# Optimization experiments

Hardware: AMD Instinct MI355X
Metric: run time of the kernel (lower is better)

Reference implementation:

```python
import jax, jax.numpy as jnp
import numpy as np

CONTEXT = 5
PAD = CONTEXT // 2
EPS = 1e-12  # torch F.normalize eps


def _conv2d(x, w, b):
    # x: [B,Cin,H,W], w: [Cout,Cin,3,3], SAME padding (pad=1)
    y = jax.lax.conv_general_dilated(
        x, w, window_strides=(1, 1), padding='SAME',
        dimension_numbers=('NCHW', 'OIHW', 'NCHW'))
    return y + b[None, :, None, None]


def _self_similarity(fn):
    # fn: L2-normalized features [B,C,H,W] -> cost volume [B,25,H,W]
    b, c, h, w = fn.shape
    fp = jnp.pad(fn, ((0, 0), (0, 0), (PAD, PAD), (PAD, PAD)))
    # channel index = col*CONTEXT + row, matching the torch loop order
    planes = [
        (fp[:, :, r:h + r, cc:w + cc] * fn).sum(axis=1)
        for cc in range(CONTEXT) for r in range(CONTEXT)
    ]
    return jnp.stack(planes, axis=1)


def setup_inputs() -> dict:
    key = jax.random.key(0)
    ks = jax.random.split(key, 5)
    B, C, H, W = 8, 512, 96, 96
    OC = 128
    return {
        'feature': jax.random.normal(ks[0], (B, C, H, W), dtype=jnp.float32),
        'w0': jax.random.normal(ks[1], (2 * OC, CONTEXT * CONTEXT, 3, 3), dtype=jnp.float32) * 0.05,
        'b0': jax.random.normal(ks[2], (2 * OC,), dtype=jnp.float32) * 0.01,
        'w1': jax.random.normal(ks[3], (OC, 2 * OC, 3, 3), dtype=jnp.float32) * 0.05,
        'b1': jax.random.normal(ks[4], (OC,), dtype=jnp.float32) * 0.01,
    }


def reference(feature, w0, b0, w1, b1):
    # F.normalize(p=2, dim=1): divide by channel L2 norm clamped to eps
    norm = jnp.sqrt((feature * feature).sum(axis=1, keepdims=True))
    fn = feature / jnp.maximum(norm, EPS)
    ss = _self_similarity(fn)                 # [B,25,H,W]
    ss1 = jax.nn.relu(_conv2d(ss, w0, b0))    # [B,256,H,W]
    ss2 = jax.nn.relu(_conv2d(ss1, w1, b1))   # [B,128,H,W]
    return jnp.concatenate((ss, ss1, ss2), axis=1)  # [B,409,H,W]
```

## Files before the change

### kernel.cpp

```cpp
#include <hip/hip_runtime.h>

#define FEAT_C 512
#define Hh 96
#define Ww 96
#define HW (Hh*Ww)
#define NB 8
#define OUTC 409

typedef __attribute__((ext_vector_type(8))) short short8;
typedef __attribute__((ext_vector_type(4))) short short4v;
typedef __attribute__((ext_vector_type(4))) float f32x4;
typedef __fp16 h2 __attribute__((ext_vector_type(2)));
typedef __fp16 h8 __attribute__((ext_vector_type(8)));

typedef __attribute__((address_space(1))) const unsigned int gu32;
typedef __attribute__((address_space(3))) unsigned int lu32;

#define VMCNT(N) do { asm volatile("s_waitcnt vmcnt(" #N ")" ::: "memory"); \
                      __builtin_amdgcn_sched_barrier(0); } while (0)
#define LGKM0()  do { asm volatile("s_waitcnt lgkmcnt(0)" ::: "memory"); \
                      __builtin_amdgcn_sched_barrier(0); } while (0)

__device__ inline ushort f2bf(float x) {
    unsigned u = __float_as_uint(x);
    u += 0x7fffu + ((u >> 16) & 1u);
    return (ushort)(u >> 16);
}

#if __has_builtin(__builtin_amdgcn_fdot2)
__device__ inline float FDOT2(h2 a, h2 b, float c) {
    return __builtin_amdgcn_fdot2(a, b, c, false);
}
#else
__device__ inline float FDOT2(h2 a, h2 b, float c) {
    return c + (float)a[0] * (float)b[0] + (float)a[1] * (float)b[1];
}
#endif

__device__ inline h2 pair(h8 v, int i) {
    switch (i) {
        case 0: return __builtin_shufflevector(v, v, 0, 1);
        case 1: return __builtin_shufflevector(v, v, 2, 3);
        case 2: return __builtin_shufflevector(v, v, 4, 5);
        default: return __builtin_shufflevector(v, v, 6, 7);
    }
}

#define PKPX 32
__global__ __launch_bounds__(256) void kpack(const float* __restrict__ f,
                                             ushort* __restrict__ fnorm) {
    __shared__ ushort tr[PKPX * 512];
    __shared__ float ssqp[8][PKPX];
    __shared__ float sinvs[PKPX];
    int tid = threadIdx.x;
    int g = tid >> 5, pl = tid & 31;
    int b = blockIdx.y;
    int p0 = blockIdx.x * PKPX;
    const float* fb = f + (size_t)b * FEAT_C * HW + p0 + pl;

    float ssq = 0.f;
#pragma unroll
    for (int q = 0; q < 8; ++q) {
        int u = g * 8 + q;
        float v[8];
#pragma unroll
        for (int j = 0; j < 8; ++j)
            v[j] = fb[(size_t)(u * 8 + j) * HW];
        h2 a0 = __builtin_amdgcn_cvt_pkrtz(v[0], v[1]);
        h2 a1 = __builtin_amdgcn_cvt_pkrtz(v[2], v[3]);
        h2 a2 = __builtin_amdgcn_cvt_pkrtz(v[4], v[5]);
        h2 a3 = __builtin_amdgcn_cvt_pkrtz(v[6], v[7]);
        ssq = FDOT2(a0, a0, ssq); ssq = FDOT2(a1, a1, ssq);
        ssq = FDOT2(a2, a2, ssq); ssq = FDOT2(a3, a3, ssq);
        h8 hv;
        hv[0] = a0[0]; hv[1] = a0[1]; hv[2] = a1[0]; hv[3] = a1[1];
        hv[4] = a2[0]; hv[5] = a2[1]; hv[6] = a3[0]; hv[7] = a3[1];
        int up = u ^ (pl & 7);
        *(h8*)&tr[pl * 512 + up * 8] = hv;
    }
    ssqp[g][pl] = ssq;
    __syncthreads();
    if (tid < PKPX) {
        float s = 0.f;
#pragma unroll
        for (int gg = 0; gg < 8; ++gg) s += ssqp[gg][tid];
        sinvs[tid] = 1.0f / fmaxf(sqrtf(s), 1e-12f);
    }
    __syncthreads();

    size_t ob = ((size_t)b * HW + p0) * 512;
#pragma unroll
    for (int i = 0; i < 8; ++i) {
        int t = tid + i * 256;
        int r = t >> 6, k = t & 63;
        h8 hv = *(const h8*)&tr[r * 512 + ((k ^ (r & 7)) * 8)];
        float s = sinvs[r];
        h2 o0 = __builtin_amdgcn_cvt_pkrtz((float)hv[0] * s, (float)hv[1] * s);
        h2 o1 = __builtin_amdgcn_cvt_pkrtz((float)hv[2] * s, (float)hv[3] * s);
        h2 o2 = __builtin_amdgcn_cvt_pkrtz((float)hv[4] * s, (float)hv[5] * s);
        h2 o3 = __builtin_amdgcn_cvt_pkrtz((float)hv[6] * s, (float)hv[7] * s);
        h8 ov;
        ov[0] = o0[0]; ov[1] = o0[1]; ov[2] = o1[0]; ov[3] = o1[1];
        ov[4] = o2[0]; ov[5] = o2[1]; ov[6] = o3[0]; ov[7] = o3[1];
        *(h8*)&fnorm[ob + (size_t)r * 512 + k * 8] = ov;
    }
}

#define SS_NPX 240
__global__ __launch_bounds__(256) void kss4(const ushort* __restrict__ fnorm,
                                            float* __restrict__ out,
                                            ushort* __restrict__ sspk0) {
    __shared__ ushort tile[2][SS_NPX * 32];
    int tid = threadIdx.x;
    int w = tid >> 6, lane = tid & 63;
    int s = lane >> 4, q = lane & 15;
    int x0 = blockIdx.x * 16, y0 = blockIdx.y * 8, b = blockIdx.z;

    size_t t_src[4];
    int t_dst[4];
    bool t_ok[4];
#pragma unroll
    for (int k = 0; k < 4; ++k) {
        int task = tid + k * 256;
        t_ok[k] = false; t_src[k] = 0; t_dst[k] = -1;
        if (task < 960) {
            int px = task >> 2, u = task & 3;
            int hr = px / 20, hc = px % 20;
            int gy = y0 + hr - 2, gx = x0 + hc - 2;
            t_dst[k] = px * 32 + ((u ^ ((px >> 1) & 3)) * 8);
            if (gy >= 0 && gy < Hh && gx >= 0 && gx < Ww) {
                t_ok[k] = true;
                t_src[k] = ((size_t)b * HW + (size_t)gy * Ww + gx) * 512 + u * 8;
            }
        }
    }

    float acc0[25], acc1[25];
#pragma unroll
    for (int o = 0; o < 25; ++o) { acc0[o] = 0.f; acc1[o] = 0.f; }

    auto stage = [&](int chunk, int nbuf) {
        short8 v[4];
#pragma unroll
        for (int k = 0; k < 4; ++k) {
            v[k] = (short8)0;
            if (t_ok[k]) v[k] = *(const short8*)(fnorm + t_src[k] + chunk * 32);
        }
#pragma unroll
        for (int k = 0; k < 4; ++k)
            if (t_dst[k] >= 0)
                *(short8*)&tile[nbuf][t_dst[k]] = v[k];
    };

    auto compute = [&](int kb) {
        const ushort* tb = tile[kb];
        auto rd = [&](int px) -> h8 {
            return *(const h8*)&tb[px * 32 + ((s ^ ((px >> 1) & 3)) * 8)];
        };
        int pc0 = (2 * w + 2) * 20 + q + 2;
        h8 c0 = rd(pc0);
        h8 c1 = rd(pc0 + 20);
#pragma unroll
        for (int dxc = 0; dxc < 5; ++dxc) {
#pragma unroll
            for (int dyr = 0; dyr < 6; ++dyr) {
                int pn = (2 * w + dyr) * 20 + q + dxc;
                h8 nv = rd(pn);
                if (dyr < 5) {
                    float a = acc0[dxc * 5 + dyr];
                    a = FDOT2(pair(nv, 0), pair(c0, 0), a);
                    a = FDOT2(pair(nv, 1), pair(c0, 1), a);
                    a = FDOT2(pair(nv, 2), pair(c0, 2), a);
                    a = FDOT2(pair(nv, 3), pair(c0, 3), a);
                    acc0[dxc * 5 + dyr] = a;
                }
                if (dyr > 0) {
                    float a = acc1[dxc * 5 + dyr - 1];
                    a = FDOT2(pair(nv, 0), pair(c1, 0), a);
                    a = FDOT2(pair(nv, 1), pair(c1, 1), a);
                    a = FDOT2(pair(nv, 2), pair(c1, 2), a);
                    a = FDOT2(pair(nv, 3), pair(c1, 3), a);
                    acc1[dxc * 5 + dyr - 1] = a;
                }
            }
        }
    };

    stage(0, 0);
    __syncthreads();
    for (int c = 0; c < 16; ++c) {
        if (c < 15) stage(c + 1, (c + 1) & 1);
        compute(c & 1);
        __syncthreads();
    }

#pragma unroll
    for (int o = 0; o < 25; ++o) {
        float v0 = acc0[o];
        v0 += __shfl_xor(v0, 16);
        v0 += __shfl_xor(v0, 32);
        acc0[o] = v0;
        float v1 = acc1[o];
        v1 += __shfl_xor(v1, 16);
        v1 += __shfl_xor(v1, 32);
        acc1[o] = v1;
    }
    if (s == 0) {
        int gy0 = y0 + 2 * w, gx = x0 + q;
        size_t pix0 = (size_t)b * HW + (size_t)gy0 * Ww + gx;
        size_t ob0 = (size_t)b * OUTC * HW + (size_t)gy0 * Ww + gx;
#pragma unroll
        for (int o = 0; o < 25; ++o) {
            out[ob0 + (size_t)o * HW] = acc0[o];
            out[ob0 + (size_t)o * HW + Ww] = acc1[o];
        }
        ushort pk0[32], pk1[32];
#pragma unroll
        for (int o = 0; o < 25; ++o) { pk0[o] = f2bf(acc0[o]); pk1[o] = f2bf(acc1[o]); }
#pragma unroll
        for (int o = 25; o < 32; ++o) { pk0[o] = 0; pk1[o] = 0; }
#pragma unroll
        for (int u = 0; u < 4; ++u) {
            *(short8*)&sspk0[pix0 * 32 + u * 8] = *(short8*)&pk0[u * 8];
            *(short8*)&sspk0[(pix0 + Ww) * 32 + u * 8] = *(short8*)&pk1[u * 8];
        }
    }
}

__global__ __launch_bounds__(256) void kwpack0(const float* __restrict__ w0,
                                               ushort* __restrict__ wpk0) {
    int i = blockIdx.x * 256 + threadIdx.x;
    if (i >= 9 * 256 * 32) return;
    int t = i >> 13, oc = (i >> 5) & 255;
    int s = (i >> 3) & 3, ii = i & 7;
    int u = s ^ ((oc >> 1) & 3);
    int ic = u * 8 + ii;
    wpk0[i] = (ic < 25) ? f2bf(w0[(size_t)oc * 225 + ic * 9 + t]) : (ushort)0;
}

__global__ __launch_bounds__(256) void kwpack1(const float* __restrict__ w1,
                                               ushort* __restrict__ wpk1,
                                               ushort* __restrict__ zpad) {
    if (blockIdx.x == 0 && threadIdx.x < 32) zpad[threadIdx.x] = 0;
    int i = blockIdx.x * 256 + threadIdx.x;
    if (i >= 8 * 9 * 128 * 32) return;
    int ct = i >> 12;
    int c = ct / 9, t = ct % 9;
    int oc = (i >> 5) & 127;
    int s = (i >> 3) & 3, ii = i & 7;
    int u = s ^ ((oc >> 1) & 3);
    int ic = c * 32 + u * 8 + ii;
    wpk1[i] = f2bf(w1[((size_t)oc * 256 + ic) * 9 + t]);
}

#define C1NPX 180
__global__ __launch_bounds__(512, 2) void kconv1m(const ushort* __restrict__ sspk0,
                                                  const ushort* __restrict__ wpk0,
                                                  const float* __restrict__ b0,
                                                  float* __restrict__ outp,
                                                  ushort* __restrict__ sspk) {
    __shared__ ushort wlds[2][8192];
    __shared__ ushort plds[C1NPX * 32];
    int tid = threadIdx.x;
    int lane = tid & 63, wid = tid >> 6;
    int wM = wid >> 1, wN = wid & 1;
    int l15 = lane & 15, l4 = lane >> 4;
    int x0 = blockIdx.x * 16, y0 = blockIdx.y * 8, b = blockIdx.z;

    auto wstage = [&](int t, int buf) {
        const ushort* src = wpk0 + (size_t)t * 8192 + wid * 1024 + lane * 8;
        ushort* dst = &wlds[buf][wid * 1024];
#pragma unroll
        for (int i = 0; i < 2; ++i)
            __builtin_amdgcn_global_load_lds((gu32*)(src + i * 512),
                                             (lu32*)(dst + i * 512), 16, 0, 0);
    };

    wstage(0, 0);

    {
        short8 v[2]; int dst[2];
#pragma unroll
        for (int k = 0; k < 2; ++k) {
            int task = tid + k * 512;
            v[k] = (short8)0; dst[k] = -1;
            if (task < 720) {
                int px = task >> 2, u = task & 3;
                int iy = px / 18, ix = px % 18;
                int gy = y0 + iy - 1, gx = x0 + ix - 1;
                dst[k] = px * 32 + (u ^ ((px >> 1) & 3)) * 8;
                if (gy >= 0 && gy < Hh && gx >= 0 && gx < Ww)
                    v[k] = *(const short8*)(sspk0 +
                            ((size_t)b * HW + (size_t)gy * Ww + gx) * 32 + u * 8);
            }
        }
#pragma unroll
        for (int k = 0; k < 2; ++k)
            if (dst[k] >= 0) *(short8*)&plds[dst[k]] = v[k];
    }
    LGKM0();
    VMCNT(0);
    __builtin_amdgcn_s_barrier();

    f32x4 acc[4][4];
#pragma unroll
    for (int mi = 0; mi < 4; ++mi)
#pragma unroll
        for (int ni = 0; ni < 4; ++ni)
            acc[mi][ni] = (f32x4)0.f;

    int wslot = l4 ^ ((l15 >> 1) & 3);
    for (int t = 0; t < 9; ++t) {
        if (t < 8) { wstage(t + 1, (t + 1) & 1); VMCNT(2); }
        else       { VMCNT(0); }
        __builtin_amdgcn_s_barrier();
        int ky = t / 3, kx = t % 3;
        const ushort* wbase = wlds[t & 1];
        short8 a[4], bv[4];
#pragma unroll
        for (int mi = 0; mi < 4; ++mi) {
            int row = wM * 64 + mi * 16 + l15;
            a[mi] = *(const short8*)&wbase[row * 32 + wslot * 8];
        }
#pragma unroll
        for (int ni = 0; ni < 4; ++ni) {
            int ipx = (wN * 4 + ni + ky) * 18 + l15 + kx;
            bv[ni] = *(const short8*)&plds[ipx * 32
                    + ((l4 ^ ((ipx >> 1) & 3)) * 8)];
        }
#pragma unroll
        for (int mi = 0; mi < 4; ++mi)
#pragma unroll
            for (int ni = 0; ni < 4; ++ni)
                acc[mi][ni] = __builtin_amdgcn_mfma_f32_16x16x32_bf16(
                    a[mi], bv[ni], acc[mi][ni], 0, 0, 0);
        LGKM0();
        __builtin_amdgcn_s_barrier();
    }

    size_t ob = (size_t)b * OUTC * HW + (size_t)25 * HW;
    size_t pb = (size_t)b * HW;
#pragma unroll
    for (int mi = 0; mi < 4; ++mi)
#pragma unroll
        for (int ni = 0; ni < 4; ++ni) {
            int gy = y0 + wN * 4 + ni, gx = x0 + l15;
            int oc_b = wM * 64 + mi * 16 + l4 * 4;
            short4v hv;
#pragma unroll
            for (int r = 0; r < 4; ++r) {
                float v = fmaxf(acc[mi][ni][r] + b0[oc_b + r], 0.f);
                outp[ob + (size_t)(oc_b + r) * HW + (size_t)gy * Ww + gx] = v;
                hv[r] = (short)f2bf(v);
            }
            *(short4v*)&sspk[(pb + (size_t)gy * Ww + gx) * 256 + oc_b] = hv;
        }
}

#define NPX2 180
__global__ __launch_bounds__(256, 2) void kconv2n(const ushort* __restrict__ sspk,
                                                  const ushort* __restrict__ wpk,
                                                  const float* __restrict__ b1,
                                                  const ushort* __restrict__ zpad,
                                                  float* __restrict__ outp) {
    __shared__ ushort plds[2][6144];
    int tid = threadIdx.x;
    int lane = tid & 63, wid = tid >> 6;
    int wM = wid >> 1, wN = wid & 1;
    int l15 = lane & 15, l4 = lane >> 4;
    int x0 = blockIdx.x * 16, y0 = blockIdx.y * 8, b = blockIdx.z;

    f32x4 acc[4][4];
#pragma unroll
    for (int mi = 0; mi < 4; ++mi)
#pragma unroll
        for (int ni = 0; ni < 4; ++ni)
            acc[mi][ni] = (f32x4)0.f;

    const ushort* p_src[3];
    int p_ok[3];
#pragma unroll
    for (int k = 0; k < 3; ++k) {
        int task = tid + k * 256;
        int px = task >> 2, slot = task & 3;
        int u = slot ^ ((px >> 1) & 3);
        int iy = px / 18, ix = px % 18;
        int gy = y0 + iy - 1, gx = x0 + ix - 1;
        bool ok = (px < NPX2) && gy >= 0 && gy < Hh && gx >= 0 && gx < Ww;
        p_ok[k] = ok ? 1 : 0;
        p_src[k] = ok ? (sspk + ((size_t)b * HW + (size_t)gy * Ww + gx) * 256
                         + u * 8)
                      : zpad;
    }
    auto pstage = [&](int c, int buf) {
#pragma unroll
        for (int k = 0; k < 3; ++k)
            __builtin_amdgcn_global_load_lds(
                (gu32*)(p_src[k] + (p_ok[k] ? c * 32 : 0)),
                (lu32*)&plds[buf][(k * 256 + wid * 64) * 8], 16, 0, 0);
    };

    int wslot = l4 ^ ((l15 >> 1) & 3);
    const ushort* abase = wpk + (size_t)(wM * 64 + l15) * 32 + wslot * 8;
    short8 sA[12], sB[12];
    auto aload = [&](int g, short8 (&S)[12]) {
#pragma unroll
        for (int kx = 0; kx < 3; ++kx)
#pragma unroll
            for (int mi = 0; mi < 4; ++mi)
                S[kx * 4 + mi] = *(const short8*)(abase + (size_t)g * 12288
                                                  + kx * 4096 + mi * 512);
    };
    auto compute = [&](const short8 (&S)[12], const ushort* lbase, int ky) {
#pragma unroll
        for (int kx = 0; kx < 3; ++kx) {
            short8 bv[4];
#pragma unroll
            for (int ni = 0; ni < 4; ++ni) {
                int oy = wN * 4 + ni;
                int ipx = (oy + ky) * 18 + l15 + kx;
                bv[ni] = *(const short8*)&lbase[ipx * 32
                        + ((l4 ^ ((ipx >> 1) & 3)) * 8)];
            }
#pragma unroll
            for (int mi = 0; mi < 4; ++mi)
#pragma unroll
                for (int ni = 0; ni < 4; ++ni)
                    acc[mi][ni] = __builtin_amdgcn_mfma_f32_16x16x32_bf16(
                        S[kx * 4 + mi], bv[ni], acc[mi][ni], 0, 0, 0);
        }
    };

    auto chunk = [&](int c, short8 (&Scur)[12], short8 (&Salt)[12], bool last) {
        const ushort* lbase = plds[c & 1];
        VMCNT(12);
        __builtin_amdgcn_s_barrier();
        compute(Scur, lbase, 0);
        aload(3 * c + 2, Scur);
        VMCNT(12);
        compute(Salt, lbase, 1);
        if (!last) {
            aload(3 * c + 3, Salt);
            pstage(c + 1, (c + 1) & 1);
            VMCNT(15);
        } else {
            VMCNT(0);
        }
        compute(Scur, lbase, 2);
        if (!last) aload(3 * c + 4, Scur);
    };

    pstage(0, 0);
    aload(0, sA);
    aload(1, sB);

    for (int c2 = 0; c2 < 4; ++c2) {
        chunk(2 * c2,     sA, sB, false);
        chunk(2 * c2 + 1, sB, sA, c2 == 3);
    }

    size_t ob = (size_t)b * OUTC * HW + (size_t)281 * HW;
#pragma unroll
    for (int mi = 0; mi < 4; ++mi)
#pragma unroll
        for (int ni = 0; ni < 4; ++ni) {
            int gy = y0 + wN * 4 + ni, gx = x0 + l15;
#pragma unroll
            for (int r = 0; r < 4; ++r) {
                int oc = wM * 64 + mi * 16 + l4 * 4 + r;
                float v = acc[mi][ni][r] + b1[oc];
                outp[ob + (size_t)oc * HW + (size_t)gy * Ww + gx] = fmaxf(v, 0.f);
            }
        }
}

extern "C" void kernel_launch(void* const* d_in, const int* in_sizes, int n_in,
                              void* d_out, int out_size, void* d_ws, size_t ws_size,
                              hipStream_t stream) {
    const float* feat = (const float*)d_in[0];
    const float* w0   = (const float*)d_in[1];
    const float* b0   = (const float*)d_in[2];
    const float* w1   = (const float*)d_in[3];
    const float* b1   = (const float*)d_in[4];
    float* out = (float*)d_out;

    ushort* wpk0  = (ushort*)d_ws;
    ushort* wpk1  = (ushort*)((char*)d_ws + 147456);
    ushort* sspk  = (ushort*)((char*)d_ws + 147456 + 589824);
    ushort* fnorm = (ushort*)((char*)d_ws + 147456 + 589824 + 37748736);
    ushort* sspk0 = (ushort*)((char*)d_ws + 147456 + 589824 + 37748736
                              + 75497472);
    ushort* zpad  = (ushort*)((char*)d_ws + 147456 + 589824 + 37748736
                              + 75497472 + 4718592);

    hipLaunchKernelGGL(kwpack0, dim3(288),  dim3(256), 0, stream, w0, wpk0);
    hipLaunchKernelGGL(kwpack1, dim3(1152), dim3(256), 0, stream, w1, wpk1, zpad);
    hipLaunchKernelGGL(kpack,   dim3(HW / PKPX, NB), dim3(256), 0, stream, feat, fnorm);
    hipLaunchKernelGGL(kss4,    dim3(6, 12, NB), dim3(256), 0, stream, fnorm, out, sspk0);
    hipLaunchKernelGGL(kconv1m, dim3(6, 12, NB), dim3(512), 0, stream, sspk0, wpk0, b0, out, sspk);
    hipLaunchKernelGGL(kconv2n, dim3(6, 12, NB), dim3(256), 0, stream, sspk, wpk1, b1, zpad, out);
}
```

Before: 195.9 us.

## Load conv1 weights directly into registers with double-buffered prefetch, dropping LDS staging

The conv1 kernel no longer stages weight tiles through shared memory with global_load_lds and per-tap barriers. Each wave now loads its A fragments straight from global memory into two register sets that alternate, prefetching two taps ahead, and the tap loop is fully unrolled with no barriers. This removes LDS traffic and nine rounds of block synchronization, and frees shared memory. In exchange it raises register pressure, and weights are re-read from global or L2 by every wave with no sharing.

```diff
diff --git a/kernel.cpp b/kernel.cpp
--- a/kernel.cpp
+++ b/kernel.cpp
@@ -259,7 +259,6 @@
                                                   const float* __restrict__ b0,
                                                   float* __restrict__ outp,
                                                   ushort* __restrict__ sspk) {
-    __shared__ ushort wlds[2][8192];
     __shared__ ushort plds[C1NPX * 32];
     int tid = threadIdx.x;
     int lane = tid & 63, wid = tid >> 6;
@@ -267,39 +266,38 @@
     int l15 = lane & 15, l4 = lane >> 4;
     int x0 = blockIdx.x * 16, y0 = blockIdx.y * 8, b = blockIdx.z;
 
-    auto wstage = [&](int t, int buf) {
-        const ushort* src = wpk0 + (size_t)t * 8192 + wid * 1024 + lane * 8;
-        ushort* dst = &wlds[buf][wid * 1024];
-#pragma unroll
-        for (int i = 0; i < 2; ++i)
-            __builtin_amdgcn_global_load_lds((gu32*)(src + i * 512),
-                                             (lu32*)(dst + i * 512), 16, 0, 0);
-    };
-
-    wstage(0, 0);
-
-    {
-        short8 v[2]; int dst[2];
-#pragma unroll
-        for (int k = 0; k < 2; ++k) {
-            int task = tid + k * 512;
-            v[k] = (short8)0; dst[k] = -1;
-            if (task < 720) {
-                int px = task >> 2, u = task & 3;
-                int iy = px / 18, ix = px % 18;
-                int gy = y0 + iy - 1, gx = x0 + ix - 1;
-                dst[k] = px * 32 + (u ^ ((px >> 1) & 3)) * 8;
-                if (gy >= 0 && gy < Hh && gx >= 0 && gx < Ww)
-                    v[k] = *(const short8*)(sspk0 +
-                            ((size_t)b * HW + (size_t)gy * Ww + gx) * 32 + u * 8);
-            }
-        }
-#pragma unroll
-        for (int k = 0; k < 2; ++k)
-            if (dst[k] >= 0) *(short8*)&plds[dst[k]] = v[k];
-    }
+    short8 pv[2]; int pdst[2];
+#pragma unroll
+    for (int k = 0; k < 2; ++k) {
+        int task = tid + k * 512;
+        pv[k] = (short8)0; pdst[k] = -1;
+        if (task < 720) {
+            int px = task >> 2, u = task & 3;
+            int iy = px / 18, ix = px % 18;
+            int gy = y0 + iy - 1, gx = x0 + ix - 1;
+            pdst[k] = px * 32 + (u ^ ((px >> 1) & 3)) * 8;
+            if (gy >= 0 && gy < Hh && gx >= 0 && gx < Ww)
+                pv[k] = *(const short8*)(sspk0 +
+                        ((size_t)b * HW + (size_t)gy * Ww + gx) * 32 + u * 8);
+        }
+    }
+
+    int wslot = l4 ^ ((l15 >> 1) & 3);
+    const ushort* abase = wpk0 + (size_t)(wM * 64 + l15) * 32 + wslot * 8;
+    short8 sA[4], sB[4];
+    auto aload = [&](int t, short8 (&S)[4]) {
+#pragma unroll
+        for (int mi = 0; mi < 4; ++mi)
+            S[mi] = *(const short8*)(abase + (size_t)t * 8192 + mi * 512);
+    };
+
+    aload(0, sA);
+    aload(1, sB);
+
+#pragma unroll
+    for (int k = 0; k < 2; ++k)
+        if (pdst[k] >= 0) *(short8*)&plds[pdst[k]] = pv[k];
     LGKM0();
-    VMCNT(0);
     __builtin_amdgcn_s_barrier();
 
     f32x4 acc[4][4];
@@ -309,19 +307,8 @@
         for (int ni = 0; ni < 4; ++ni)
             acc[mi][ni] = (f32x4)0.f;
 
-    int wslot = l4 ^ ((l15 >> 1) & 3);
-    for (int t = 0; t < 9; ++t) {
-        if (t < 8) { wstage(t + 1, (t + 1) & 1); VMCNT(2); }
-        else       { VMCNT(0); }
-        __builtin_amdgcn_s_barrier();
-        int ky = t / 3, kx = t % 3;
-        const ushort* wbase = wlds[t & 1];
-        short8 a[4], bv[4];
-#pragma unroll
-        for (int mi = 0; mi < 4; ++mi) {
-            int row = wM * 64 + mi * 16 + l15;
-            a[mi] = *(const short8*)&wbase[row * 32 + wslot * 8];
-        }
+    auto compute = [&](const short8 (&S)[4], int ky, int kx) {
+        short8 bv[4];
 #pragma unroll
         for (int ni = 0; ni < 4; ++ni) {
             int ipx = (wN * 4 + ni + ky) * 18 + l15 + kx;
@@ -333,9 +320,20 @@
 #pragma unroll
             for (int ni = 0; ni < 4; ++ni)
                 acc[mi][ni] = __builtin_amdgcn_mfma_f32_16x16x32_bf16(
-                    a[mi], bv[ni], acc[mi][ni], 0, 0, 0);
-        LGKM0();
-        __builtin_amdgcn_s_barrier();
+                    S[mi], bv[ni], acc[mi][ni], 0, 0, 0);
+    };
+
+#pragma unroll
+    for (int t = 0; t < 9; ++t) {
+        if (t < 8) { VMCNT(4); } else { VMCNT(0); }
+        int ky = t / 3, kx = t % 3;
+        if ((t & 1) == 0) {
+            compute(sA, ky, kx);
+            if (t < 7) aload(t + 2, sA);
+        } else {
+            compute(sB, ky, kx);
+            if (t < 7) aload(t + 2, sB);
+        }
     }
 
     size_t ob = (size_t)b * OUTC * HW + (size_t)25 * HW;
```

Result: faster. 191.8 us (-2.1%).
